# Kernel tuning notes

Measured on AMD Instinct MI355X. Metric: run time of the kernel, lower is better.

Reference implementation:

```python
import jax, jax.numpy as jnp
import numpy as np

B, S, D, F, A, H, O = 8, 2048, 64, 16, 32, 4, 64
HD = A // H  # head dim = 8
TWO_PI = 2.0 * np.pi


def setup_inputs() -> dict:
    key = jax.random.key(0)
    ks = jax.random.split(key, 10)
    sc = lambda k, sh, fan: (jax.random.normal(k, sh, jnp.float32) / np.sqrt(fan)).astype(jnp.float32)
    Din = D + 2 * D * F  # input width to gate/projection MLPs
    return dict(
        x=jax.random.normal(ks[0], (B, S, D), jnp.float32),
        freq_matrix=jnp.tile(jnp.linspace(1.0, 10.0, F, dtype=jnp.float32)[None, :], (D, 1)),
        phase=jax.random.normal(ks[1], (D, F), jnp.float32),
        freq_scale=jnp.ones((D, F), jnp.float32),
        Wq=sc(ks[2], (A, D), D), bq=jnp.zeros((A,), jnp.float32),          # query_proj
        Wk1=sc(ks[3], (A, 1), 1), bk1=jnp.zeros((A,), jnp.float32),        # key_proj (Linear(1, A))
        Wqi=sc(ks[4], (A, A), A), bqi=jnp.zeros((A,), jnp.float32),        # MHA in-proj (q slice)
        Wki=sc(ks[5], (A, A), A), bki=jnp.zeros((A,), jnp.float32),        # MHA in-proj (k slice)
        Wg=sc(ks[6], (O, Din), Din), bg=jnp.zeros((O,), jnp.float32),      # gate linear
        Wp=sc(ks[7], (O, Din), Din), bp=jnp.zeros((O,), jnp.float32),      # projection linear
    )


def reference(x, freq_matrix, phase, freq_scale, Wq, bq, Wk1, bk1, Wqi, bqi, Wki, bki, Wg, bg, Wp, bp):
    # x: [B, S, D]
    t = jnp.linspace(0.0, 1.0, S, dtype=x.dtype)                 # [S]
    f = freq_matrix * freq_scale                                 # [D, F]
    # fourier signal, batched over all input dims at once
    signal = TWO_PI * t[:, None, None] * f[None] + phase[None]   # [S, D, F]
    sin_f, cos_f = jnp.sin(signal), jnp.cos(signal)

    # MHA attention weights (averaged over heads) -- attn_out is discarded by the module
    queries = jnp.einsum('bsd,ad->bsa', x, Wq) + bq              # [B, S, A]
    q = (jnp.einsum('bsa,ea->bse', queries, Wqi) + bqi).reshape(B, S, H, HD)
    keys = f[:, :, None] * Wk1[None, None, :, 0] + bk1           # [D, F, A] via Linear(1, A)
    k = (jnp.einsum('dfa,ea->dfe', keys, Wki) + bki).reshape(D, F, H, HD)
    scores = jnp.einsum('bshe,dfhe->bdhsf', q, k) / np.sqrt(HD)  # [B, D, H, S, F]
    attn = jax.nn.softmax(scores, axis=-1).mean(axis=2)          # [B, D, S, F] (head-avg)
    aw = jnp.transpose(attn, (0, 2, 1, 3))                       # [B, S, D, F]

    # weighted fourier features; per-dim layout is [sin(F), cos(F)] to match torch cat order
    ff = jnp.concatenate([sin_f[None] * aw, cos_f[None] * aw], axis=-1)  # [B, S, D, 2F]
    ff = ff.reshape(B, S, D * 2 * F)

    ci = jnp.concatenate([x, ff], axis=-1)                       # [B, S, D + 2DF]
    gated = jax.nn.sigmoid(jnp.einsum('bsi,oi->bso', ci, Wg) + bg) * \
            jax.nn.silu(jnp.einsum('bsi,oi->bso', ci, Wp) + bp)
    return x + gated
```

## Files before the change

### kernel.cpp

```cpp
#include <hip/hip_runtime.h>
#include <math.h>

#define SS 2048
#define DIN 2112
#define NKT 66
#define TOK 16
#define NBLK 1024
#define NTHR 256
#define ASTR 264
#define XSTR 68
#define CSTR 132
#define BFRAG_ELEMS (NKT * 8 * 64 * 8)
#define LOG2E 1.4426950408889634f
#define INV2PI 0.15915494309189535f

#define OFF_WP 135168
#define OFF_CP 135424
#define OFF_FV 135680
#define OFF_PH 136192
#define OFF_MX 136704

typedef __attribute__((ext_vector_type(4))) float f32x4;
typedef __attribute__((ext_vector_type(8))) _Float16 f16x8;
typedef __attribute__((ext_vector_type(2))) __fp16 fp16v2;

__device__ __forceinline__ unsigned pkh(float a, float b) {
#if __has_builtin(__builtin_amdgcn_cvt_pkrtz)
    union { fp16v2 h; unsigned u; } r;
    r.h = __builtin_amdgcn_cvt_pkrtz(a, b);
    return r.u;
#else
    union { _Float16 h[2]; unsigned u; } r;
    r.h[0] = (_Float16)a; r.h[1] = (_Float16)b;
    return r.u;
#endif
}

#if __has_builtin(__builtin_amdgcn_exp2f)
#define EXP2(x) __builtin_amdgcn_exp2f(x)
#else
#define EXP2(x) exp2f(x)
#endif
#if __has_builtin(__builtin_amdgcn_rcpf)
#define RCP(x) __builtin_amdgcn_rcpf(x)
#else
#define RCP(x) (1.0f / (x))
#endif
#if __has_builtin(__builtin_amdgcn_sinf)
#define SINR(x) __builtin_amdgcn_sinf(x)
#define COSR(x) __builtin_amdgcn_cosf(x)
#else
#define SINR(x) __sinf(6.283185307179586f * (x))
#define COSR(x) __cosf(6.283185307179586f * (x))
#endif

__global__ __launch_bounds__(256) void aff_pre(
    const float* __restrict__ Wq, const float* __restrict__ bq,
    const float* __restrict__ Wk1,
    const float* __restrict__ Wqi, const float* __restrict__ bqi,
    const float* __restrict__ Wki,
    const float* __restrict__ Wg, const float* __restrict__ Wp,
    const float* __restrict__ fm, const float* __restrict__ fs,
    const float* __restrict__ phase,
    float* __restrict__ ws)
{
    _Float16* Bf = (_Float16*)ws;
    const int tid = threadIdx.x;
    const int gid = blockIdx.x * 256 + tid;

    {
        int j  = gid & 7;
        int q  = (gid >> 3) & 3;
        int nl = (gid >> 5) & 15;
        int nt = (gid >> 9) & 7;
        int kt = gid >> 12;
        int k = kt * 32 + q * 8 + j;
        int n = nt * 16 + nl;
        float s = (n < 64) ? Wg[(size_t)n * DIN + k] : Wp[(size_t)(n - 64) * DIN + k];
        int dst = ((kt * 8 + nt) * 64 + q * 16 + nl) * 8 + j;
        Bf[dst] = (_Float16)s;
    }

    if (blockIdx.x == 0) {
        float* WP = ws + OFF_WP;
        float* cP = ws + OFF_CP;
        unsigned* fvh = (unsigned*)(ws + OFF_FV);
        unsigned* phh = (unsigned*)(ws + OFF_PH);
        float* mxg = ws + OFF_MX;

        {
            float4 a = ((const float4*)fm)[tid];
            float4 b = ((const float4*)fs)[tid];
            fvh[tid * 2]     = pkh(a.x * b.x, a.y * b.y);
            fvh[tid * 2 + 1] = pkh(a.z * b.z, a.w * b.w);
            float4 p = ((const float4*)phase)[tid];
            phh[tid * 2]     = pkh(p.x * INV2PI, p.y * INV2PI);
            phh[tid * 2 + 1] = pkh(p.z * INV2PI, p.w * INV2PI);
        }
        if (tid < 64) {
            float mx = -1e30f, mn = 1e30f;
            #pragma unroll
            for (int f = 0; f < 16; ++f) {
                float v = (float)(_Float16)(fm[tid * 16 + f] * fs[tid * 16 + f]);
                mx = fmaxf(mx, v); mn = fminf(mn, v);
            }
            mxg[tid * 2] = mx; mxg[tid * 2 + 1] = mn;
        }

        __shared__ float u[32];
        if (tid < 32) {
            float s = 0.f;
            #pragma unroll
            for (int a = 0; a < 32; ++a) s += Wki[tid * 32 + a] * Wk1[a];
            u[tid] = s;
        }
        __syncthreads();
        {
            const int h = tid >> 6;
            const int d = tid & 63;
            float s = 0.f;
            for (int j = 0; j < 8; ++j) {
                int e = h * 8 + j;
                float wc = 0.f;
                #pragma unroll
                for (int a = 0; a < 32; ++a) wc += Wqi[e * 32 + a] * Wq[a * 64 + d];
                s += u[e] * wc;
            }
            WP[h * 64 + d] = s * 0.35355339059327373f * LOG2E;
            if (d == 0) {
                float sc = 0.f;
                for (int j = 0; j < 8; ++j) {
                    int e = h * 8 + j;
                    float bcv = bqi[e];
                    #pragma unroll
                    for (int a = 0; a < 32; ++a) bcv += Wqi[e * 32 + a] * bq[a];
                    sc += u[e] * bcv;
                }
                cP[h] = sc * 0.35355339059327373f * LOG2E;
            }
        }
    }
}

__global__ __launch_bounds__(NTHR, 6) void aff_main(
    const float* __restrict__ x,
    const float* __restrict__ ws_c,
    const float* __restrict__ bg, const float* __restrict__ bp,
    float* __restrict__ out)
{
    __shared__ __align__(16) float xs[TOK * XSTR];
    __shared__ __align__(16) _Float16 Ab[2][TOK * ASTR];
    __shared__ __align__(16) float Pl[TOK * 4];
    __shared__ __align__(16) _Float16 fvh[1024];
    __shared__ __align__(16) _Float16 phh[1024];
    __shared__ __align__(16) float mxs[128];

    const f16x8* Bv = (const f16x8*)ws_c;
    const float* WP  = ws_c + OFF_WP;
    const float* cP  = ws_c + OFF_CP;
    const float* mxg = ws_c + OFF_MX;

    const int tid  = threadIdx.x;
    const int lane = tid & 63;
    const int w    = tid >> 6;
    const int t0   = blockIdx.x * TOK;
    const int lm   = lane & 15;
    const int lq   = lane >> 4;
    const int fh   = lq & 1;
    const int dsel = lane >> 5;
    const int dloc = (w << 1) + dsel;

    {
        uint2 fv2 = ((const uint2*)(ws_c + OFF_FV))[tid];
        uint2 ph2 = ((const uint2*)(ws_c + OFF_PH))[tid];
        ((uint2*)fvh)[tid] = fv2;
        ((uint2*)phh)[tid] = ph2;
    }
    if (tid < 32) ((float4*)mxs)[tid] = ((const float4*)mxg)[tid];
    {
        int t = tid >> 4, j4 = (tid & 15) * 4;
        float4 xv = *(const float4*)(x + (size_t)(t0 + t) * 64 + j4);
        *(float4*)(xs + t * XSTR + j4) = xv;
    }
    __syncthreads();

    if (tid < 128) {
        int t = tid & 15, dh = (tid >> 4) & 1, h = tid >> 5;
        float acc = 0.f;
        const float* wp = WP + h * 64 + dh * 32;
        const float* xr = xs + t * XSTR + dh * 32;
        #pragma unroll 8
        for (int d = 0; d < 32; ++d) acc = fmaf(wp[d], xr[d], acc);
        acc += __shfl_xor(acc, 16);
        if (dh == 0) Pl[t * 4 + h] = acc + cP[h];
    }

    f32x4 acc0 = {}, acc1 = {};

    #pragma unroll
    for (int ks = 0; ks < 2; ++ks) {
        f16x8 b0 = Bv[((size_t)ks * 8 + 2 * w) * 64 + lane];
        f16x8 b1 = Bv[((size_t)ks * 8 + 2 * w + 1) * 64 + lane];
        const float* xr = xs + lm * XSTR + ks * 32 + lq * 8;
        float4 fa = *(const float4*)xr;
        float4 fb = *(const float4*)(xr + 4);
        union { unsigned u[4]; f16x8 v; } av;
        av.u[0] = pkh(fa.x, fa.y); av.u[1] = pkh(fa.z, fa.w);
        av.u[2] = pkh(fb.x, fb.y); av.u[3] = pkh(fb.z, fb.w);
        acc0 = __builtin_amdgcn_mfma_f32_16x16x32_f16(av.v, b0, acc0, 0, 0, 0);
        acc1 = __builtin_amdgcn_mfma_f32_16x16x32_f16(av.v, b1, acc1, 0, 0, 0);
    }
    __syncthreads();

    const float w2 = (float)((t0 + lm) & (SS - 1)) * (1.0f / 2047.0f);

    const _Float16* fvp0 = fvh + dloc * 16 + fh * 8;
    const _Float16* php0 = phh + dloc * 16 + fh * 8;
    const float* mxp0 = mxs + dloc * 2;
    _Float16* dst0 = &Ab[0][lm * ASTR + dloc * 32 + fh * 8];
    _Float16* dst1 = &Ab[1][lm * ASTR + dloc * 32 + fh * 8];

    auto build = [&](int ch, _Float16* dst) {
        union { uint4 q; _Float16 h[8]; } fu, pu;
        fu.q = *(const uint4*)(fvp0 + ch * 128);
        pu.q = *(const uint4*)(php0 + ch * 128);
        const float4 Pv = *(const float4*)(Pl + lm * 4);
        const float mxv = mxp0[ch * 16], mnv = mxp0[ch * 16 + 1];
        float fl[8], pr[8];
        #pragma unroll
        for (int j = 0; j < 8; ++j) { fl[j] = (float)fu.h[j]; pr[j] = (float)pu.h[j]; }
        float aw[8] = {0.f, 0.f, 0.f, 0.f, 0.f, 0.f, 0.f, 0.f};
        float Ph4[4] = {Pv.x, Pv.y, Pv.z, Pv.w};
        #pragma unroll
        for (int h = 0; h < 4; ++h) {
            float Ph = Ph4[h];
            float m = fmaxf(mxv * Ph, mnv * Ph);
            float e[8]; float s = 0.f;
            #pragma unroll
            for (int j = 0; j < 8; ++j) { e[j] = EXP2(fmaf(fl[j], Ph, -m)); s += e[j]; }
            float z = s + __shfl_xor(s, 16);
            float inv = 0.25f * RCP(z);
            #pragma unroll
            for (int j = 0; j < 8; ++j) aw[j] = fmaf(e[j], inv, aw[j]);
        }
        unsigned sv[4], cv[4];
        #pragma unroll
        for (int jp = 0; jp < 4; ++jp) {
            int j0 = 2 * jp;
            float X0 = fmaf(w2, fl[j0], pr[j0]);
            float X1 = fmaf(w2, fl[j0 + 1], pr[j0 + 1]);
            float a0 = aw[j0], a1 = aw[j0 + 1];
            sv[jp] = pkh(a0 * SINR(X0), a1 * SINR(X1));
            cv[jp] = pkh(a0 * COSR(X0), a1 * COSR(X1));
        }
        uint4 v0; v0.x = sv[0]; v0.y = sv[1]; v0.z = sv[2]; v0.w = sv[3];
        uint4 v1; v1.x = cv[0]; v1.y = cv[1]; v1.z = cv[2]; v1.w = cv[3];
        *(uint4*)dst = v0;
        *(uint4*)(dst + 16) = v1;
    };

    build(0, dst0);
    __syncthreads();

    for (int ch = 0; ch < 8; ++ch) {
        const _Float16* Ar = &Ab[ch & 1][0];
        #pragma unroll
        for (int ks = 0; ks < 8; ++ks) {
            const size_t kt = (size_t)(2 + ch * 8 + ks);
            f16x8 b0 = Bv[(kt * 8 + 2 * w) * 64 + lane];
            f16x8 b1 = Bv[(kt * 8 + 2 * w + 1) * 64 + lane];
            f16x8 a = *(const f16x8*)(Ar + lm * ASTR + ks * 32 + lq * 8);
            acc0 = __builtin_amdgcn_mfma_f32_16x16x32_f16(a, b0, acc0, 0, 0, 0);
            acc1 = __builtin_amdgcn_mfma_f32_16x16x32_f16(a, b1, acc1, 0, 0, 0);
        }
        if (ch < 7) build(ch + 1, (ch & 1) ? dst0 : dst1);
        __syncthreads();
    }

    float* Cb = (float*)(&Ab[0][0]);
    #pragma unroll
    for (int r = 0; r < 4; ++r) {
        Cb[(lq * 4 + r) * CSTR + (2 * w) * 16 + lm]     = acc0[r];
        Cb[(lq * 4 + r) * CSTR + (2 * w + 1) * 16 + lm] = acc1[r];
    }
    __syncthreads();
    {
        int t = tid >> 4, o0 = (tid & 15) * 4;
        float4 g4 = *(float4*)(Cb + t * CSTR + o0);
        float4 p4 = *(float4*)(Cb + t * CSTR + 64 + o0);
        float4 bg4 = *(const float4*)(bg + o0);
        float4 bp4 = *(const float4*)(bp + o0);
        float4 xr = *(float4*)(xs + t * XSTR + o0);
        float4 o;
        { float g = g4.x + bg4.x, p = p4.x + bp4.x;
          float sg = RCP(1.f + EXP2(-g * LOG2E));
          float sp = RCP(1.f + EXP2(-p * LOG2E));
          o.x = fmaf(p * sg, sp, xr.x); }
        { float g = g4.y + bg4.y, p = p4.y + bp4.y;
          float sg = RCP(1.f + EXP2(-g * LOG2E));
          float sp = RCP(1.f + EXP2(-p * LOG2E));
          o.y = fmaf(p * sg, sp, xr.y); }
        { float g = g4.z + bg4.z, p = p4.z + bp4.z;
          float sg = RCP(1.f + EXP2(-g * LOG2E));
          float sp = RCP(1.f + EXP2(-p * LOG2E));
          o.z = fmaf(p * sg, sp, xr.z); }
        { float g = g4.w + bg4.w, p = p4.w + bp4.w;
          float sg = RCP(1.f + EXP2(-g * LOG2E));
          float sp = RCP(1.f + EXP2(-p * LOG2E));
          o.w = fmaf(p * sg, sp, xr.w); }
        *(float4*)(out + (size_t)(t0 + t) * 64 + o0) = o;
    }
}

extern "C" void kernel_launch(void* const* d_in, const int* in_sizes, int n_in,
                              void* d_out, int out_size, void* d_ws, size_t ws_size,
                              hipStream_t stream) {
    (void)in_sizes; (void)n_in; (void)out_size; (void)ws_size;
    const float* x    = (const float*)d_in[0];
    const float* fm   = (const float*)d_in[1];
    const float* phs  = (const float*)d_in[2];
    const float* fs   = (const float*)d_in[3];
    const float* Wq   = (const float*)d_in[4];
    const float* bq   = (const float*)d_in[5];
    const float* Wk1  = (const float*)d_in[6];
    const float* Wqi  = (const float*)d_in[8];
    const float* bqi  = (const float*)d_in[9];
    const float* Wki  = (const float*)d_in[10];
    const float* Wg   = (const float*)d_in[12];
    const float* bg   = (const float*)d_in[13];
    const float* Wp   = (const float*)d_in[14];
    const float* bp   = (const float*)d_in[15];
    float* out = (float*)d_out;
    float* ws  = (float*)d_ws;

    aff_pre<<<BFRAG_ELEMS / 256, 256, 0, stream>>>(Wq, bq, Wk1, Wqi, bqi, Wki, Wg, Wp,
                                                   fm, fs, phs, ws);
    aff_main<<<NBLK, NTHR, 0, stream>>>(x, (const float*)ws, bg, bp, out);
}
```

Before: 121.4 us.

## Split K across waves with register-resident A fragments and per-wave partial sums

Each wave now owns a slice of 16 input dims (split-K) instead of a slice of output columns. It builds the attention-weighted fourier A fragment straight in registers and accumulates all 8 output tiles. The lane layout is changed so cos is computed as sin with a quarter-turn phase offset and heads are split across lane halves via a shuffle. This removes the shared-memory A staging and the per-chunk block barriers. The cost is a larger shared-memory reduction of four partial C tiles, more accumulator and B registers (occupancy hint lowered from 6 to 3), and a double-buffered B prefetch from global.

```diff
diff --git a/kernel.cpp b/kernel.cpp
--- a/kernel.cpp
+++ b/kernel.cpp
@@ -3,14 +3,12 @@
 
 #define SS 2048
 #define DIN 2112
-#define NKT 66
 #define TOK 16
 #define NBLK 1024
 #define NTHR 256
-#define ASTR 264
 #define XSTR 68
 #define CSTR 132
-#define BFRAG_ELEMS (NKT * 8 * 64 * 8)
+#define BFRAG_ELEMS (66 * 8 * 64 * 8)
 #define LOG2E 1.4426950408889634f
 #define INV2PI 0.15915494309189535f
 
@@ -48,10 +46,8 @@
 #endif
 #if __has_builtin(__builtin_amdgcn_sinf)
 #define SINR(x) __builtin_amdgcn_sinf(x)
-#define COSR(x) __builtin_amdgcn_cosf(x)
 #else
 #define SINR(x) __sinf(6.283185307179586f * (x))
-#define COSR(x) __cosf(6.283185307179586f * (x))
 #endif
 
 __global__ __launch_bounds__(256) void aff_pre(
@@ -142,14 +138,14 @@
     }
 }
 
-__global__ __launch_bounds__(NTHR, 6) void aff_main(
+__global__ __launch_bounds__(NTHR, 3) void aff_main(
     const float* __restrict__ x,
     const float* __restrict__ ws_c,
     const float* __restrict__ bg, const float* __restrict__ bp,
     float* __restrict__ out)
 {
     __shared__ __align__(16) float xs[TOK * XSTR];
-    __shared__ __align__(16) _Float16 Ab[2][TOK * ASTR];
+    __shared__ __align__(16) float Cpart[4 * TOK * CSTR];
     __shared__ __align__(16) float Pl[TOK * 4];
     __shared__ __align__(16) _Float16 fvh[1024];
     __shared__ __align__(16) _Float16 phh[1024];
@@ -166,9 +162,9 @@
     const int t0   = blockIdx.x * TOK;
     const int lm   = lane & 15;
     const int lq   = lane >> 4;
-    const int fh   = lq & 1;
-    const int dsel = lane >> 5;
-    const int dloc = (w << 1) + dsel;
+    const int fsel = lq & 1;
+    const int hp   = lq >> 1;
+    const float qoff = hp ? 0.25f : 0.0f;
 
     {
         uint2 fv2 = ((const uint2*)(ws_c + OFF_FV))[tid];
@@ -184,8 +180,9 @@
     }
     __syncthreads();
 
-    if (tid < 128) {
-        int t = tid & 15, dh = (tid >> 4) & 1, h = tid >> 5;
+    if (tid >= 128) {
+        int t2 = tid - 128;
+        int t = t2 & 15, dh = (t2 >> 4) & 1, h = t2 >> 5;
         float acc = 0.f;
         const float* wp = WP + h * 64 + dh * 32;
         const float* xr = xs + t * XSTR + dh * 32;
@@ -195,119 +192,111 @@
         if (dh == 0) Pl[t * 4 + h] = acc + cP[h];
     }
 
-    f32x4 acc0 = {}, acc1 = {};
+    f32x4 acc[8] = {};
+    f16x8 B0[8], B1[8];
+    auto loadB = [&](int kt, f16x8* Bb) {
+        const f16x8* p = Bv + (size_t)kt * 512 + lane;
+        #pragma unroll
+        for (int nt = 0; nt < 8; ++nt) Bb[nt] = p[nt * 64];
+    };
+
+    const int dbase = w * 16;
+
+    if (w < 2) {
+        loadB(w, B0);
+        union { unsigned u[4]; f16x8 v; } ax;
+        const float* xr = xs + lm * XSTR + w * 32 + lq * 8;
+        ax.u[0] = pkh(xr[0], xr[1]); ax.u[1] = pkh(xr[2], xr[3]);
+        ax.u[2] = pkh(xr[4], xr[5]); ax.u[3] = pkh(xr[6], xr[7]);
+        loadB(2 + dbase, B1);
+        #pragma unroll
+        for (int nt = 0; nt < 8; ++nt)
+            acc[nt] = __builtin_amdgcn_mfma_f32_16x16x32_f16(ax.v, B0[nt], acc[nt], 0, 0, 0);
+    } else {
+        loadB(2 + dbase, B1);
+    }
+    __syncthreads();
+
+    const float P0 = Pl[lm * 4 + hp * 2];
+    const float P1 = Pl[lm * 4 + hp * 2 + 1];
+    const float w2 = (float)((t0 + lm) & (SS - 1)) * (1.0f / 2047.0f);
+
+    auto build = [&](int d) -> f16x8 {
+        union { uint4 q; _Float16 h[8]; } fu, pu;
+        fu.q = *(const uint4*)(fvh + d * 16 + fsel * 8);
+        pu.q = *(const uint4*)(phh + d * 16 + fsel * 8);
+        const float mxv = mxs[d * 2], mnv = mxs[d * 2 + 1];
+        float fl[8], prq[8];
+        #pragma unroll
+        for (int j = 0; j < 8; ++j) { fl[j] = (float)fu.h[j]; prq[j] = (float)pu.h[j] + qoff; }
+        const float m0 = fmaxf(mxv * P0, mnv * P0);
+        const float m1 = fmaxf(mxv * P1, mnv * P1);
+        float e0[8], e1[8], s0 = 0.f, s1 = 0.f;
+        #pragma unroll
+        for (int j = 0; j < 8; ++j) { e0[j] = EXP2(fmaf(fl[j], P0, -m0)); s0 += e0[j]; }
+        #pragma unroll
+        for (int j = 0; j < 8; ++j) { e1[j] = EXP2(fmaf(fl[j], P1, -m1)); s1 += e1[j]; }
+        const float z0 = s0 + __shfl_xor(s0, 16);
+        const float z1 = s1 + __shfl_xor(s1, 16);
+        const float i0 = 0.25f * RCP(z0), i1 = 0.25f * RCP(z1);
+        union { unsigned u[4]; f16x8 v; } r;
+        #pragma unroll
+        for (int jp = 0; jp < 4; ++jp) {
+            const int j0 = 2 * jp, j1 = 2 * jp + 1;
+            float a0 = fmaf(e1[j0], i1, e0[j0] * i0);
+            float a1 = fmaf(e1[j1], i1, e0[j1] * i0);
+            a0 += __shfl_xor(a0, 32);
+            a1 += __shfl_xor(a1, 32);
+            const float X0 = fmaf(w2, fl[j0], prq[j0]);
+            const float X1 = fmaf(w2, fl[j1], prq[j1]);
+            r.u[jp] = pkh(a0 * SINR(X0), a1 * SINR(X1));
+        }
+        return r.v;
+    };
 
     #pragma unroll
-    for (int ks = 0; ks < 2; ++ks) {
-        f16x8 b0 = Bv[((size_t)ks * 8 + 2 * w) * 64 + lane];
-        f16x8 b1 = Bv[((size_t)ks * 8 + 2 * w + 1) * 64 + lane];
-        const float* xr = xs + lm * XSTR + ks * 32 + lq * 8;
-        float4 fa = *(const float4*)xr;
-        float4 fb = *(const float4*)(xr + 4);
-        union { unsigned u[4]; f16x8 v; } av;
-        av.u[0] = pkh(fa.x, fa.y); av.u[1] = pkh(fa.z, fa.w);
-        av.u[2] = pkh(fb.x, fb.y); av.u[3] = pkh(fb.z, fb.w);
-        acc0 = __builtin_amdgcn_mfma_f32_16x16x32_f16(av.v, b0, acc0, 0, 0, 0);
-        acc1 = __builtin_amdgcn_mfma_f32_16x16x32_f16(av.v, b1, acc1, 0, 0, 0);
+    for (int i = 0; i < 16; ++i) {
+        f16x8* cur = (i & 1) ? B0 : B1;
+        f16x8* nxt = (i & 1) ? B1 : B0;
+        f16x8 a = build(dbase + i);
+        if (i < 15) loadB(2 + dbase + i + 1, nxt);
+        #pragma unroll
+        for (int nt = 0; nt < 8; ++nt)
+            acc[nt] = __builtin_amdgcn_mfma_f32_16x16x32_f16(a, cur[nt], acc[nt], 0, 0, 0);
+    }
+
+    {
+        float* Cw = Cpart + w * TOK * CSTR;
+        #pragma unroll
+        for (int nt = 0; nt < 8; ++nt)
+            #pragma unroll
+            for (int r = 0; r < 4; ++r)
+                Cw[(lq * 4 + r) * CSTR + nt * 16 + lm] = acc[nt][r];
     }
     __syncthreads();
-
-    const float w2 = (float)((t0 + lm) & (SS - 1)) * (1.0f / 2047.0f);
-
-    const _Float16* fvp0 = fvh + dloc * 16 + fh * 8;
-    const _Float16* php0 = phh + dloc * 16 + fh * 8;
-    const float* mxp0 = mxs + dloc * 2;
-    _Float16* dst0 = &Ab[0][lm * ASTR + dloc * 32 + fh * 8];
-    _Float16* dst1 = &Ab[1][lm * ASTR + dloc * 32 + fh * 8];
-
-    auto build = [&](int ch, _Float16* dst) {
-        union { uint4 q; _Float16 h[8]; } fu, pu;
-        fu.q = *(const uint4*)(fvp0 + ch * 128);
-        pu.q = *(const uint4*)(php0 + ch * 128);
-        const float4 Pv = *(const float4*)(Pl + lm * 4);
-        const float mxv = mxp0[ch * 16], mnv = mxp0[ch * 16 + 1];
-        float fl[8], pr[8];
-        #pragma unroll
-        for (int j = 0; j < 8; ++j) { fl[j] = (float)fu.h[j]; pr[j] = (float)pu.h[j]; }
-        float aw[8] = {0.f, 0.f, 0.f, 0.f, 0.f, 0.f, 0.f, 0.f};
-        float Ph4[4] = {Pv.x, Pv.y, Pv.z, Pv.w};
-        #pragma unroll
-        for (int h = 0; h < 4; ++h) {
-            float Ph = Ph4[h];
-            float m = fmaxf(mxv * Ph, mnv * Ph);
-            float e[8]; float s = 0.f;
-            #pragma unroll
-            for (int j = 0; j < 8; ++j) { e[j] = EXP2(fmaf(fl[j], Ph, -m)); s += e[j]; }
-            float z = s + __shfl_xor(s, 16);
-            float inv = 0.25f * RCP(z);
-            #pragma unroll
-            for (int j = 0; j < 8; ++j) aw[j] = fmaf(e[j], inv, aw[j]);
-        }
-        unsigned sv[4], cv[4];
-        #pragma unroll
-        for (int jp = 0; jp < 4; ++jp) {
-            int j0 = 2 * jp;
-            float X0 = fmaf(w2, fl[j0], pr[j0]);
-            float X1 = fmaf(w2, fl[j0 + 1], pr[j0 + 1]);
-            float a0 = aw[j0], a1 = aw[j0 + 1];
-            sv[jp] = pkh(a0 * SINR(X0), a1 * SINR(X1));
-            cv[jp] = pkh(a0 * COSR(X0), a1 * COSR(X1));
-        }
-        uint4 v0; v0.x = sv[0]; v0.y = sv[1]; v0.z = sv[2]; v0.w = sv[3];
-        uint4 v1; v1.x = cv[0]; v1.y = cv[1]; v1.z = cv[2]; v1.w = cv[3];
-        *(uint4*)dst = v0;
-        *(uint4*)(dst + 16) = v1;
-    };
-
-    build(0, dst0);
-    __syncthreads();
-
-    for (int ch = 0; ch < 8; ++ch) {
-        const _Float16* Ar = &Ab[ch & 1][0];
-        #pragma unroll
-        for (int ks = 0; ks < 8; ++ks) {
-            const size_t kt = (size_t)(2 + ch * 8 + ks);
-            f16x8 b0 = Bv[(kt * 8 + 2 * w) * 64 + lane];
-            f16x8 b1 = Bv[(kt * 8 + 2 * w + 1) * 64 + lane];
-            f16x8 a = *(const f16x8*)(Ar + lm * ASTR + ks * 32 + lq * 8);
-            acc0 = __builtin_amdgcn_mfma_f32_16x16x32_f16(a, b0, acc0, 0, 0, 0);
-            acc1 = __builtin_amdgcn_mfma_f32_16x16x32_f16(a, b1, acc1, 0, 0, 0);
-        }
-        if (ch < 7) build(ch + 1, (ch & 1) ? dst0 : dst1);
-        __syncthreads();
-    }
-
-    float* Cb = (float*)(&Ab[0][0]);
-    #pragma unroll
-    for (int r = 0; r < 4; ++r) {
-        Cb[(lq * 4 + r) * CSTR + (2 * w) * 16 + lm]     = acc0[r];
-        Cb[(lq * 4 + r) * CSTR + (2 * w + 1) * 16 + lm] = acc1[r];
-    }
-    __syncthreads();
     {
         int t = tid >> 4, o0 = (tid & 15) * 4;
-        float4 g4 = *(float4*)(Cb + t * CSTR + o0);
-        float4 p4 = *(float4*)(Cb + t * CSTR + 64 + o0);
+        float4 g4 = make_float4(0.f, 0.f, 0.f, 0.f), p4 = g4;
+        #pragma unroll
+        for (int ww = 0; ww < 4; ++ww) {
+            const float* Cw = Cpart + ww * TOK * CSTR + t * CSTR;
+            float4 g = *(const float4*)(Cw + o0);
+            float4 p = *(const float4*)(Cw + 64 + o0);
+            g4.x += g.x; g4.y += g.y; g4.z += g.z; g4.w += g.w;
+            p4.x += p.x; p4.y += p.y; p4.z += p.z; p4.w += p.w;
+        }
         float4 bg4 = *(const float4*)(bg + o0);
         float4 bp4 = *(const float4*)(bp + o0);
         float4 xr = *(float4*)(xs + t * XSTR + o0);
         float4 o;
         { float g = g4.x + bg4.x, p = p4.x + bp4.x;
-          float sg = RCP(1.f + EXP2(-g * LOG2E));
-          float sp = RCP(1.f + EXP2(-p * LOG2E));
-          o.x = fmaf(p * sg, sp, xr.x); }
+          o.x = fmaf(p * RCP(1.f + EXP2(-g * LOG2E)), RCP(1.f + EXP2(-p * LOG2E)), xr.x); }
         { float g = g4.y + bg4.y, p = p4.y + bp4.y;
-          float sg = RCP(1.f + EXP2(-g * LOG2E));
-          float sp = RCP(1.f + EXP2(-p * LOG2E));
-          o.y = fmaf(p * sg, sp, xr.y); }
+          o.y = fmaf(p * RCP(1.f + EXP2(-g * LOG2E)), RCP(1.f + EXP2(-p * LOG2E)), xr.y); }
         { float g = g4.z + bg4.z, p = p4.z + bp4.z;
-          float sg = RCP(1.f + EXP2(-g * LOG2E));
-          float sp = RCP(1.f + EXP2(-p * LOG2E));
-          o.z = fmaf(p * sg, sp, xr.z); }
+          o.z = fmaf(p * RCP(1.f + EXP2(-g * LOG2E)), RCP(1.f + EXP2(-p * LOG2E)), xr.z); }
         { float g = g4.w + bg4.w, p = p4.w + bp4.w;
-          float sg = RCP(1.f + EXP2(-g * LOG2E));
-          float sp = RCP(1.f + EXP2(-p * LOG2E));
-          o.w = fmaf(p * sg, sp, xr.w); }
+          o.w = fmaf(p * RCP(1.f + EXP2(-g * LOG2E)), RCP(1.f + EXP2(-p * LOG2E)), xr.w); }
         *(float4*)(out + (size_t)(t0 + t) * 64 + o0) = o;
     }
 }
```

Result: no change. 122.4 us (+0.9%).
